# Kernel optimization log

Hardware: AMD Instinct MI355X
Metric: run time of the kernel (lower is better)

Reference implementation:

```python
import jax, jax.numpy as jnp
import numpy as np

N_SRC = 100000
N_DST = 100000
N_EDGES = 640000
D = 128
D_OUT = 128


def setup_inputs() -> dict:
    key = jax.random.key(0)
    k1, k2, k3, k4, k5, k6 = jax.random.split(key, 6)
    h_src = jax.random.normal(k1, (N_SRC, D), dtype=jnp.float32)
    h_dst = jax.random.normal(k2, (N_DST, D), dtype=jnp.float32)
    src_idx = jax.random.randint(k3, (N_EDGES,), 0, N_SRC, dtype=jnp.int32)
    dst_idx = jax.random.randint(k4, (N_EDGES,), 0, N_DST, dtype=jnp.int32)
    W = jax.random.normal(k5, (2 * D, D_OUT), dtype=jnp.float32) * 0.05
    b = jax.random.normal(k6, (D_OUT,), dtype=jnp.float32) * 0.05
    return {"h_src": h_src, "h_dst": h_dst, "src_idx": src_idx,
            "dst_idx": dst_idx, "W": W, "b": b}


def reference(h_src, h_dst, src_idx, dst_idx, W, b):
    # copy_u: gather source features along edges -> [E, D]
    msgs = h_src[src_idx]
    # mean aggregation per destination node (segment mean)
    summed = jax.ops.segment_sum(msgs, dst_idx, num_segments=N_DST)  # [N_dst, D]
    deg = jax.ops.segment_sum(jnp.ones((N_EDGES,), dtype=h_src.dtype),
                              dst_idx, num_segments=N_DST)  # [N_dst]
    h_N = summed / jnp.maximum(deg, 1.0)[:, None]
    # concat self + neighbor mean, then linear projection
    h_total = jnp.concatenate([h_dst, h_N], axis=1)  # [N_dst, 2D]
    return h_total @ W + b
```

## Files before the change

kernel.cpp:

```cpp
#include <hip/hip_runtime.h>

#define D 128
#define N_SRC 100000
#define N_DST 100000
#define N_EDGES 640000

#define SCAN_BLK 1024
#define N_SCAN_BLOCKS ((N_DST + SCAN_BLK - 1) / SCAN_BLK)

#define HIST_BLOCKS ((N_EDGES + 255) / 256)
#define CVT_BLOCKS  ((N_SRC * D / 8) / 256)
#define PACKW_BLOCKS 128

typedef __attribute__((ext_vector_type(8))) short s8v;
typedef __attribute__((ext_vector_type(4))) float f32x4;

__device__ __forceinline__ unsigned short f2bf(float f) {
    unsigned int u = __float_as_uint(f);
    u += 0x7fffu + ((u >> 16) & 1u);
    return (unsigned short)(u >> 16);
}

__device__ __forceinline__ unsigned int pk2(float a, float b) {
    return (unsigned int)f2bf(a) | ((unsigned int)f2bf(b) << 16);
}

__global__ __launch_bounds__(256) void prep(
    const int* __restrict__ dst_idx, int* __restrict__ counts,
    const float* __restrict__ h_src, unsigned int* __restrict__ A32,
    const float* __restrict__ W, unsigned short* __restrict__ Bp)
{
    const int blk = blockIdx.x;
    const int tid = threadIdx.x;
    if (blk < HIST_BLOCKS) {
        int e = blk * 256 + tid;
        if (e < N_EDGES) atomicAdd(&counts[dst_idx[e]], 1);
    } else if (blk < HIST_BLOCKS + CVT_BLOCKS) {
        int id = (blk - HIST_BLOCKS) * 256 + tid;
        size_t e = (size_t)id * 8;
        const float4* p = (const float4*)(h_src + e);
        float4 x = p[0], y = p[1];
        uint4 o;
        o.x = pk2(x.x, x.y); o.y = pk2(x.z, x.w);
        o.z = pk2(y.x, y.y); o.w = pk2(y.z, y.w);
        int r = id >> 4;
        int c = (id & 15) * 8;
        *(uint4*)(A32 + (size_t)r * 128 + (c >> 1)) = o;
    } else {
        int id = (blk - HIST_BLOCKS - CVT_BLOCKS) * 256 + tid;
        if (id < 32768) {
            int j = id & 7;
            int l = (id >> 3) & 63;
            int t = (id >> 9) & 7;
            int s = id >> 12;
            int k = s * 32 + (l >> 4) * 8 + j;
            int n = t * 16 + (l & 15);
            Bp[id] = f2bf(W[k * D + n]);
        }
    }
}


__global__ __launch_bounds__(256) void scan_blocks(
    const int* __restrict__ counts, int* __restrict__ row_start,
    int* __restrict__ block_sums)
{
    __shared__ int sh[256];
    const int tid = threadIdx.x;
    const int base = blockIdx.x * SCAN_BLK + tid * 4;
    int v[4];
    int local = 0;
#pragma unroll
    for (int k = 0; k < 4; k++) {
        int idx = base + k;
        v[k] = (idx < N_DST) ? counts[idx] : 0;
        local += v[k];
    }
    sh[tid] = local;
    __syncthreads();
    for (int off = 1; off < 256; off <<= 1) {
        int t = (tid >= off) ? sh[tid - off] : 0;
        __syncthreads();
        sh[tid] += t;
        __syncthreads();
    }
    int run = (tid == 0) ? 0 : sh[tid - 1];
    if (tid == 255) block_sums[blockIdx.x] = sh[255];
#pragma unroll
    for (int k = 0; k < 4; k++) {
        int idx = base + k;
        if (idx < N_DST) row_start[idx] = run;
        run += v[k];
    }
}

__global__ __launch_bounds__(256) void add_offsets(
    int* __restrict__ row_start, const int* __restrict__ block_sums,
    int* __restrict__ cursor)
{
    __shared__ int sh[128];
    const int tid = threadIdx.x;
    if (tid < 128) sh[tid] = (tid < N_SCAN_BLOCKS) ? block_sums[tid] : 0;
    __syncthreads();
    for (int off = 1; off < 128; off <<= 1) {
        int t = (tid < 128 && tid >= off) ? sh[tid - off] : 0;
        __syncthreads();
        if (tid < 128) sh[tid] += t;
        __syncthreads();
    }
    int i = blockIdx.x * 256 + tid;
    if (i < N_DST) {
        int blk = i / SCAN_BLK;
        int off = (blk == 0) ? 0 : sh[blk - 1];
        int v = row_start[i] + off;
        row_start[i] = v;
        cursor[i] = v;
    }
    if (i == 0) row_start[N_DST] = N_EDGES;
}

__global__ __launch_bounds__(256) void scatter_perm(
    const int* __restrict__ src_idx, const int* __restrict__ dst_idx,
    int* __restrict__ cursor, int* __restrict__ edge_src)
{
    int e = blockIdx.x * 256 + threadIdx.x;
    if (e < N_EDGES) {
        int d = dst_idx[e];
        int pos = atomicAdd(&cursor[d], 1);
        edge_src[pos] = src_idx[e];
    }
}

__global__ __launch_bounds__(256) void aggregate(
    const unsigned short* __restrict__ hs16,
    const int* __restrict__ row_start,
    const int* __restrict__ edge_src, unsigned int* __restrict__ A32)
{
    const int wave = threadIdx.x >> 6;
    const int half = (threadIdx.x >> 5) & 1;
    const int hl = threadIdx.x & 31;
    const int row = blockIdx.x * 8 + wave * 2 + half;
    const int start = row_start[row];
    const int deg = row_start[row + 1] - start;
    f32x4 acc = {0.f, 0.f, 0.f, 0.f};
    for (int base = 0; base < deg; base += 8) {
        int j = base + (hl & 7);
        int myid = edge_src[start + min(j, deg - 1)];
#pragma unroll
        for (int t = 0; t < 8; t++) {
            int s = __shfl(myid, t, 32);
            uint2 u = *(const uint2*)(hs16 + (size_t)s * 256 + hl * 4);
            float m = ((base + t) < deg) ? 1.f : 0.f;
            acc.x = fmaf(__uint_as_float(u.x << 16), m, acc.x);
            acc.y = fmaf(__uint_as_float(u.x & 0xffff0000u), m, acc.y);
            acc.z = fmaf(__uint_as_float(u.y << 16), m, acc.z);
            acc.w = fmaf(__uint_as_float(u.y & 0xffff0000u), m, acc.w);
        }
    }
    const float inv = 1.0f / fmaxf((float)deg, 1.0f);
    uint2 o;
    o.x = pk2(acc.x * inv, acc.y * inv);
    o.y = pk2(acc.z * inv, acc.w * inv);
    *(uint2*)(A32 + (size_t)row * 128 + 64 + hl * 2) = o;
}

__global__ __launch_bounds__(256, 4) void mfma_gemm(
    const float* __restrict__ h_dst,
    const unsigned short* __restrict__ A,
    const unsigned short* __restrict__ Bp,
    const float* __restrict__ bias,
    float* __restrict__ out)
{
    const int wave = threadIdx.x >> 6;
    const int lane = threadIdx.x & 63;
    const int row0 = (blockIdx.x * 4 + wave) * 16;
    if (row0 >= N_DST) return;
    const int quad = lane >> 4;
    const int lr = lane & 15;
    const int r0 = row0 + lr;

    const float* p0 = h_dst + (size_t)r0 * D + quad * 8;
    const unsigned short* q0 = A + (size_t)r0 * 256 + 128 + quad * 8;

    float4 x[4], y[4];
    s8v an[4];
#pragma unroll
    for (int s = 0; s < 4; s++) {
        x[s] = *(const float4*)(p0 + s * 32);
        y[s] = *(const float4*)(p0 + s * 32 + 4);
        an[s] = *(const s8v*)(q0 + s * 32);
    }

    f32x4 acc[8];
#pragma unroll
    for (int t = 0; t < 8; t++) acc[t] = (f32x4){0.f, 0.f, 0.f, 0.f};

#pragma unroll
    for (int s = 0; s < 8; s++) {
        s8v a0;
        if (s < 4) {
            unsigned short au[8];
            au[0] = f2bf(x[s].x); au[1] = f2bf(x[s].y);
            au[2] = f2bf(x[s].z); au[3] = f2bf(x[s].w);
            au[4] = f2bf(y[s].x); au[5] = f2bf(y[s].y);
            au[6] = f2bf(y[s].z); au[7] = f2bf(y[s].w);
            a0 = *(s8v*)au;
        } else {
            a0 = an[s - 4];
        }
#pragma unroll
        for (int t = 0; t < 8; t++) {
            s8v bf = *(const s8v*)(Bp + ((size_t)(s * 8 + t) * 64 + lane) * 8);
            acc[t] = __builtin_amdgcn_mfma_f32_16x16x32_bf16(a0, bf, acc[t], 0, 0, 0);
        }
    }

#pragma unroll
    for (int t = 0; t < 8; t++) {
        float bv = bias[t * 16 + lr];
#pragma unroll
        for (int r = 0; r < 4; r++) {
            int rowa = row0 + quad * 4 + r;
            out[(size_t)rowa * D + t * 16 + lr] = acc[t][r] + bv;
        }
    }
}

extern "C" void kernel_launch(void* const* d_in, const int* in_sizes, int n_in,
                              void* d_out, int out_size, void* d_ws, size_t ws_size,
                              hipStream_t stream) {
    const float* h_src  = (const float*)d_in[0];
    const float* h_dst  = (const float*)d_in[1];
    const int* src_idx  = (const int*)d_in[2];
    const int* dst_idx  = (const int*)d_in[3];
    const float* W      = (const float*)d_in[4];
    const float* b      = (const float*)d_in[5];
    float* out = (float*)d_out;

    unsigned short* Bp = (unsigned short*)d_ws;
    int* ws_i          = (int*)((char*)d_ws + 65536);
    int* row_start     = ws_i;
    int* cursor        = row_start + (N_DST + 1);
    int* counts        = cursor + N_DST;
    int* block_sums    = counts + N_DST;
    int* edge_src      = block_sums + N_SCAN_BLOCKS;

    hipMemsetAsync(counts, 0, (size_t)N_DST * sizeof(int), stream);

    prep<<<HIST_BLOCKS + CVT_BLOCKS + PACKW_BLOCKS, 256, 0, stream>>>(
        dst_idx, counts, h_src, (unsigned int*)d_out, W, Bp);

    scan_blocks<<<N_SCAN_BLOCKS, 256, 0, stream>>>(counts, row_start, block_sums);
    add_offsets<<<(N_DST + 255) / 256, 256, 0, stream>>>(row_start, block_sums, cursor);
    scatter_perm<<<(N_EDGES + 255) / 256, 256, 0, stream>>>(src_idx, dst_idx, cursor, edge_src);

    aggregate<<<N_DST / 8, 256, 0, stream>>>(
        (const unsigned short*)d_out, row_start, edge_src, (unsigned int*)d_out);

    int gemm_blocks = (N_DST / 16 + 3) / 4;
    mfma_gemm<<<gemm_blocks, 256, 0, stream>>>(
        h_dst, (const unsigned short*)d_out, Bp, b, out);
}
```

Measured before the change: 263.8 us.

## Widen aggregate loads to 16 bytes and keep weight fragments in registers

The aggregate kernel now gives each destination row 16 lanes that each load 8 bf16 values per neighbor, instead of 32 lanes loading 4, so gathers use wider loads and each block covers 16 rows. The GEMM is reorganized so each block covers 64 rows and each wave owns two output column tiles. Each wave loads its slice of the packed weights into registers once, rather than re-reading the full 64KB of packed weights per 16-row tile. The cost is that all four waves in a block read the same h_dst and aggregate rows, and a __syncthreads is added because the output buffer aliases the aggregate input. The occupancy hint is lowered to fit the larger register footprint.

```diff
diff --git a/kernel.cpp b/kernel.cpp
--- a/kernel.cpp
+++ b/kernel.cpp
@@ -137,34 +137,40 @@
     const int* __restrict__ edge_src, unsigned int* __restrict__ A32)
 {
     const int wave = threadIdx.x >> 6;
-    const int half = (threadIdx.x >> 5) & 1;
-    const int hl = threadIdx.x & 31;
-    const int row = blockIdx.x * 8 + wave * 2 + half;
+    const int grp = (threadIdx.x >> 4) & 3;
+    const int gl = threadIdx.x & 15;
+    const int row = blockIdx.x * 16 + wave * 4 + grp;
     const int start = row_start[row];
     const int deg = row_start[row + 1] - start;
-    f32x4 acc = {0.f, 0.f, 0.f, 0.f};
+    float acc[8] = {0.f, 0.f, 0.f, 0.f, 0.f, 0.f, 0.f, 0.f};
     for (int base = 0; base < deg; base += 8) {
-        int j = base + (hl & 7);
+        int j = base + (gl & 7);
         int myid = edge_src[start + min(j, deg - 1)];
 #pragma unroll
         for (int t = 0; t < 8; t++) {
-            int s = __shfl(myid, t, 32);
-            uint2 u = *(const uint2*)(hs16 + (size_t)s * 256 + hl * 4);
+            int s = __shfl(myid, t, 16);
+            uint4 u = *(const uint4*)(hs16 + (size_t)s * 256 + gl * 8);
             float m = ((base + t) < deg) ? 1.f : 0.f;
-            acc.x = fmaf(__uint_as_float(u.x << 16), m, acc.x);
-            acc.y = fmaf(__uint_as_float(u.x & 0xffff0000u), m, acc.y);
-            acc.z = fmaf(__uint_as_float(u.y << 16), m, acc.z);
-            acc.w = fmaf(__uint_as_float(u.y & 0xffff0000u), m, acc.w);
+            acc[0] = fmaf(__uint_as_float(u.x << 16), m, acc[0]);
+            acc[1] = fmaf(__uint_as_float(u.x & 0xffff0000u), m, acc[1]);
+            acc[2] = fmaf(__uint_as_float(u.y << 16), m, acc[2]);
+            acc[3] = fmaf(__uint_as_float(u.y & 0xffff0000u), m, acc[3]);
+            acc[4] = fmaf(__uint_as_float(u.z << 16), m, acc[4]);
+            acc[5] = fmaf(__uint_as_float(u.z & 0xffff0000u), m, acc[5]);
+            acc[6] = fmaf(__uint_as_float(u.w << 16), m, acc[6]);
+            acc[7] = fmaf(__uint_as_float(u.w & 0xffff0000u), m, acc[7]);
         }
     }
     const float inv = 1.0f / fmaxf((float)deg, 1.0f);
-    uint2 o;
-    o.x = pk2(acc.x * inv, acc.y * inv);
-    o.y = pk2(acc.z * inv, acc.w * inv);
-    *(uint2*)(A32 + (size_t)row * 128 + 64 + hl * 2) = o;
-}
-
-__global__ __launch_bounds__(256, 4) void mfma_gemm(
+    uint4 o;
+    o.x = pk2(acc[0] * inv, acc[1] * inv);
+    o.y = pk2(acc[2] * inv, acc[3] * inv);
+    o.z = pk2(acc[4] * inv, acc[5] * inv);
+    o.w = pk2(acc[6] * inv, acc[7] * inv);
+    *(uint4*)(A32 + (size_t)row * 128 + 64 + gl * 4) = o;
+}
+
+__global__ __launch_bounds__(256, 3) void mfma_gemm(
     const float* __restrict__ h_dst,
     const unsigned short* __restrict__ A,
     const unsigned short* __restrict__ Bp,
@@ -173,55 +179,71 @@
 {
     const int wave = threadIdx.x >> 6;
     const int lane = threadIdx.x & 63;
-    const int row0 = (blockIdx.x * 4 + wave) * 16;
-    if (row0 >= N_DST) return;
     const int quad = lane >> 4;
     const int lr = lane & 15;
-    const int r0 = row0 + lr;
-
-    const float* p0 = h_dst + (size_t)r0 * D + quad * 8;
-    const unsigned short* q0 = A + (size_t)r0 * 256 + 128 + quad * 8;
-
-    float4 x[4], y[4];
-    s8v an[4];
-#pragma unroll
-    for (int s = 0; s < 4; s++) {
-        x[s] = *(const float4*)(p0 + s * 32);
-        y[s] = *(const float4*)(p0 + s * 32 + 4);
-        an[s] = *(const s8v*)(q0 + s * 32);
-    }
-
-    f32x4 acc[8];
-#pragma unroll
-    for (int t = 0; t < 8; t++) acc[t] = (f32x4){0.f, 0.f, 0.f, 0.f};
-
-#pragma unroll
-    for (int s = 0; s < 8; s++) {
-        s8v a0;
-        if (s < 4) {
-            unsigned short au[8];
-            au[0] = f2bf(x[s].x); au[1] = f2bf(x[s].y);
-            au[2] = f2bf(x[s].z); au[3] = f2bf(x[s].w);
-            au[4] = f2bf(y[s].x); au[5] = f2bf(y[s].y);
-            au[6] = f2bf(y[s].z); au[7] = f2bf(y[s].w);
-            a0 = *(s8v*)au;
-        } else {
-            a0 = an[s - 4];
-        }
-#pragma unroll
-        for (int t = 0; t < 8; t++) {
-            s8v bf = *(const s8v*)(Bp + ((size_t)(s * 8 + t) * 64 + lane) * 8);
-            acc[t] = __builtin_amdgcn_mfma_f32_16x16x32_bf16(a0, bf, acc[t], 0, 0, 0);
-        }
-    }
-
-#pragma unroll
-    for (int t = 0; t < 8; t++) {
-        float bv = bias[t * 16 + lr];
+    const int row0 = blockIdx.x * 64;
+    const int t0 = wave * 2;
+
+    s8v Bf[8][2];
+#pragma unroll
+    for (int s = 0; s < 8; s++)
+#pragma unroll
+        for (int j = 0; j < 2; j++)
+            Bf[s][j] = *(const s8v*)(Bp + ((size_t)(s * 8 + t0 + j) * 64 + lane) * 8);
+
+    f32x4 acc[4][2];
+#pragma unroll
+    for (int rg = 0; rg < 4; rg++)
+#pragma unroll
+        for (int j = 0; j < 2; j++)
+            acc[rg][j] = (f32x4){0.f, 0.f, 0.f, 0.f};
+
+#pragma unroll
+    for (int rg = 0; rg < 4; rg++) {
+        int r = row0 + rg * 16 + lr;
+        int rc = min(r, N_DST - 1);
+        const float* p = h_dst + (size_t)rc * D + quad * 8;
+        const unsigned short* q = A + (size_t)rc * 256 + 128 + quad * 8;
+
+        float4 x[4], y[4];
+        s8v an[4];
+#pragma unroll
+        for (int s = 0; s < 4; s++) {
+            x[s] = *(const float4*)(p + s * 32);
+            y[s] = *(const float4*)(p + s * 32 + 4);
+            an[s] = *(const s8v*)(q + s * 32);
+        }
+#pragma unroll
+        for (int s = 0; s < 8; s++) {
+            s8v a0;
+            if (s < 4) {
+                unsigned short au[8];
+                au[0] = f2bf(x[s].x); au[1] = f2bf(x[s].y);
+                au[2] = f2bf(x[s].z); au[3] = f2bf(x[s].w);
+                au[4] = f2bf(y[s].x); au[5] = f2bf(y[s].y);
+                au[6] = f2bf(y[s].z); au[7] = f2bf(y[s].w);
+                a0 = *(s8v*)au;
+            } else {
+                a0 = an[s - 4];
+            }
+            acc[rg][0] = __builtin_amdgcn_mfma_f32_16x16x32_bf16(a0, Bf[s][0], acc[rg][0], 0, 0, 0);
+            acc[rg][1] = __builtin_amdgcn_mfma_f32_16x16x32_bf16(a0, Bf[s][1], acc[rg][1], 0, 0, 0);
+        }
+    }
+
+    __syncthreads();
+
+    float bv0 = bias[t0 * 16 + lr];
+    float bv1 = bias[(t0 + 1) * 16 + lr];
+#pragma unroll
+    for (int rg = 0; rg < 4; rg++) {
 #pragma unroll
         for (int r = 0; r < 4; r++) {
-            int rowa = row0 + quad * 4 + r;
-            out[(size_t)rowa * D + t * 16 + lr] = acc[t][r] + bv;
+            int row = row0 + rg * 16 + quad * 4 + r;
+            if (row < N_DST) {
+                out[(size_t)row * D + t0 * 16 + lr] = acc[rg][0][r] + bv0;
+                out[(size_t)row * D + (t0 + 1) * 16 + lr] = acc[rg][1][r] + bv1;
+            }
         }
     }
 }
@@ -254,10 +276,10 @@
     add_offsets<<<(N_DST + 255) / 256, 256, 0, stream>>>(row_start, block_sums, cursor);
     scatter_perm<<<(N_EDGES + 255) / 256, 256, 0, stream>>>(src_idx, dst_idx, cursor, edge_src);
 
-    aggregate<<<N_DST / 8, 256, 0, stream>>>(
+    aggregate<<<N_DST / 16, 256, 0, stream>>>(
         (const unsigned short*)d_out, row_start, edge_src, (unsigned int*)d_out);
 
-    int gemm_blocks = (N_DST / 16 + 3) / 4;
+    int gemm_blocks = (N_DST + 63) / 64;
     mfma_gemm<<<gemm_blocks, 256, 0, stream>>>(
         h_dst, (const unsigned short*)d_out, Bp, b, out);
 }
```

Measured after the change: 279.3 us. 1.06x slower.

## Fuse neighbor aggregation into MFMA GEMM via swizzled LDS tile

Applied to the files above, without the earlier changes.

Merges the aggregate and GEMM kernels into a single kernel. Each 128-thread block computes bf16 neighbor means for 32 rows into a swizzled shared-memory tile, then feeds them straight to the MFMA projection, so the aggregated rows no longer go out to global memory and come back. The bf16 copy of h_src now sits in a compact 256-byte-per-row workspace buffer instead of being interleaved in the output buffer, and each lane gathers 16 bytes per edge. The trade-off is that blocks are smaller and each block serializes its gather phase before the matmul, which may limit how well the two phases overlap.

```diff
diff --git a/kernel.cpp b/kernel.cpp
--- a/kernel.cpp
+++ b/kernel.cpp
@@ -27,7 +27,7 @@
 
 __global__ __launch_bounds__(256) void prep(
     const int* __restrict__ dst_idx, int* __restrict__ counts,
-    const float* __restrict__ h_src, unsigned int* __restrict__ A32,
+    const float* __restrict__ h_src, unsigned int* __restrict__ mir32,
     const float* __restrict__ W, unsigned short* __restrict__ Bp)
 {
     const int blk = blockIdx.x;
@@ -43,9 +43,7 @@
         uint4 o;
         o.x = pk2(x.x, x.y); o.y = pk2(x.z, x.w);
         o.z = pk2(y.x, y.y); o.w = pk2(y.z, y.w);
-        int r = id >> 4;
-        int c = (id & 15) * 8;
-        *(uint4*)(A32 + (size_t)r * 128 + (c >> 1)) = o;
+        *(uint4*)(mir32 + (size_t)(id >> 4) * 64 + (id & 15) * 4) = o;
     } else {
         int id = (blk - HIST_BLOCKS - CVT_BLOCKS) * 256 + tid;
         if (id < 32768) {
@@ -131,64 +129,85 @@
     }
 }
 
-__global__ __launch_bounds__(256) void aggregate(
-    const unsigned short* __restrict__ hs16,
+__global__ __launch_bounds__(128, 4) void fused_ag(
+    const float* __restrict__ h_dst,
+    const unsigned short* __restrict__ mir,
     const int* __restrict__ row_start,
-    const int* __restrict__ edge_src, unsigned int* __restrict__ A32)
-{
-    const int wave = threadIdx.x >> 6;
-    const int half = (threadIdx.x >> 5) & 1;
-    const int hl = threadIdx.x & 31;
-    const int row = blockIdx.x * 8 + wave * 2 + half;
-    const int start = row_start[row];
-    const int deg = row_start[row + 1] - start;
-    f32x4 acc = {0.f, 0.f, 0.f, 0.f};
-    for (int base = 0; base < deg; base += 8) {
-        int j = base + (hl & 7);
-        int myid = edge_src[start + min(j, deg - 1)];
-#pragma unroll
-        for (int t = 0; t < 8; t++) {
-            int s = __shfl(myid, t, 32);
-            uint2 u = *(const uint2*)(hs16 + (size_t)s * 256 + hl * 4);
-            float m = ((base + t) < deg) ? 1.f : 0.f;
-            acc.x = fmaf(__uint_as_float(u.x << 16), m, acc.x);
-            acc.y = fmaf(__uint_as_float(u.x & 0xffff0000u), m, acc.y);
-            acc.z = fmaf(__uint_as_float(u.y << 16), m, acc.z);
-            acc.w = fmaf(__uint_as_float(u.y & 0xffff0000u), m, acc.w);
-        }
-    }
-    const float inv = 1.0f / fmaxf((float)deg, 1.0f);
-    uint2 o;
-    o.x = pk2(acc.x * inv, acc.y * inv);
-    o.y = pk2(acc.z * inv, acc.w * inv);
-    *(uint2*)(A32 + (size_t)row * 128 + 64 + hl * 2) = o;
-}
-
-__global__ __launch_bounds__(256, 4) void mfma_gemm(
-    const float* __restrict__ h_dst,
-    const unsigned short* __restrict__ A,
+    const int* __restrict__ edge_src,
     const unsigned short* __restrict__ Bp,
     const float* __restrict__ bias,
     float* __restrict__ out)
 {
-    const int wave = threadIdx.x >> 6;
-    const int lane = threadIdx.x & 63;
-    const int row0 = (blockIdx.x * 4 + wave) * 16;
-    if (row0 >= N_DST) return;
+    __shared__ uint4 hN4[512];
+    char* hN = (char*)hN4;
+
+    const int tid = threadIdx.x;
+    const int wave = tid >> 6;
+    const int lane = tid & 63;
     const int quad = lane >> 4;
     const int lr = lane & 15;
-    const int r0 = row0 + lr;
-
+    const int rw0 = blockIdx.x * 32 + wave * 16;
+
+#pragma unroll
+    for (int i = 0; i < 4; i++) {
+        int rl = wave * 16 + i * 4 + quad;
+        int row = blockIdx.x * 32 + rl;
+        int start = row_start[row];
+        int deg = row_start[row + 1] - start;
+        float a[8] = {0.f, 0.f, 0.f, 0.f, 0.f, 0.f, 0.f, 0.f};
+        for (int base = 0; base < deg; base += 8) {
+            int j = base + (lr & 7);
+            int myid = edge_src[start + min(j, deg - 1)];
+#pragma unroll
+            for (int t = 0; t < 8; t++) {
+                int s = __shfl(myid, t, 16);
+                uint4 u = *(const uint4*)(mir + (size_t)s * 128 + lr * 8);
+                float m = ((base + t) < deg) ? 1.f : 0.f;
+                a[0] = fmaf(__uint_as_float(u.x << 16), m, a[0]);
+                a[1] = fmaf(__uint_as_float(u.x & 0xffff0000u), m, a[1]);
+                a[2] = fmaf(__uint_as_float(u.y << 16), m, a[2]);
+                a[3] = fmaf(__uint_as_float(u.y & 0xffff0000u), m, a[3]);
+                a[4] = fmaf(__uint_as_float(u.z << 16), m, a[4]);
+                a[5] = fmaf(__uint_as_float(u.z & 0xffff0000u), m, a[5]);
+                a[6] = fmaf(__uint_as_float(u.w << 16), m, a[6]);
+                a[7] = fmaf(__uint_as_float(u.w & 0xffff0000u), m, a[7]);
+            }
+        }
+        float inv = 1.0f / fmaxf((float)deg, 1.0f);
+        uint4 o;
+        o.x = pk2(a[0] * inv, a[1] * inv);
+        o.y = pk2(a[2] * inv, a[3] * inv);
+        o.z = pk2(a[4] * inv, a[5] * inv);
+        o.w = pk2(a[6] * inv, a[7] * inv);
+        int ba = (rl * 256 + lr * 16) ^ ((rl & 7) << 4);
+        *(uint4*)(hN + ba) = o;
+    }
+
+    s8v an[4];
+    {
+        int rl = wave * 16 + lr;
+#pragma unroll
+        for (int s = 0; s < 4; s++) {
+            int ba = (rl * 256 + s * 64 + quad * 16) ^ ((rl & 7) << 4);
+            an[s] = *(const s8v*)(hN + ba);
+        }
+    }
+
+    const int r0 = rw0 + lr;
     const float* p0 = h_dst + (size_t)r0 * D + quad * 8;
-    const unsigned short* q0 = A + (size_t)r0 * 256 + 128 + quad * 8;
-
-    float4 x[4], y[4];
-    s8v an[4];
+    float4 x0[4], y0[4];
 #pragma unroll
     for (int s = 0; s < 4; s++) {
-        x[s] = *(const float4*)(p0 + s * 32);
-        y[s] = *(const float4*)(p0 + s * 32 + 4);
-        an[s] = *(const s8v*)(q0 + s * 32);
+        x0[s] = *(const float4*)(p0 + s * 32);
+        y0[s] = *(const float4*)(p0 + s * 32 + 4);
+    }
+    s8v af0[4];
+#pragma unroll
+    for (int s = 0; s < 4; s++) {
+        unsigned short u0[8];
+        u0[0]=f2bf(x0[s].x); u0[1]=f2bf(x0[s].y); u0[2]=f2bf(x0[s].z); u0[3]=f2bf(x0[s].w);
+        u0[4]=f2bf(y0[s].x); u0[5]=f2bf(y0[s].y); u0[6]=f2bf(y0[s].z); u0[7]=f2bf(y0[s].w);
+        af0[s] = *(s8v*)u0;
     }
 
     f32x4 acc[8];
@@ -197,17 +216,7 @@
 
 #pragma unroll
     for (int s = 0; s < 8; s++) {
-        s8v a0;
-        if (s < 4) {
-            unsigned short au[8];
-            au[0] = f2bf(x[s].x); au[1] = f2bf(x[s].y);
-            au[2] = f2bf(x[s].z); au[3] = f2bf(x[s].w);
-            au[4] = f2bf(y[s].x); au[5] = f2bf(y[s].y);
-            au[6] = f2bf(y[s].z); au[7] = f2bf(y[s].w);
-            a0 = *(s8v*)au;
-        } else {
-            a0 = an[s - 4];
-        }
+        s8v a0 = (s < 4) ? af0[s] : an[s - 4];
 #pragma unroll
         for (int t = 0; t < 8; t++) {
             s8v bf = *(const s8v*)(Bp + ((size_t)(s * 8 + t) * 64 + lane) * 8);
@@ -220,8 +229,8 @@
         float bv = bias[t * 16 + lr];
 #pragma unroll
         for (int r = 0; r < 4; r++) {
-            int rowa = row0 + quad * 4 + r;
-            out[(size_t)rowa * D + t * 16 + lr] = acc[t][r] + bv;
+            int row = rw0 + quad * 4 + r;
+            out[(size_t)row * D + t * 16 + lr] = acc[t][r] + bv;
         }
     }
 }
@@ -245,19 +254,18 @@
     int* block_sums    = counts + N_DST;
     int* edge_src      = block_sums + N_SCAN_BLOCKS;
 
+    size_t int_bytes = (size_t)(N_DST + 1 + N_DST + N_DST + N_SCAN_BLOCKS + N_EDGES) * 4;
+    size_t mir_off   = (65536 + int_bytes + 255) & ~(size_t)255;
+    unsigned short* mir = (unsigned short*)((char*)d_ws + mir_off);
+
     hipMemsetAsync(counts, 0, (size_t)N_DST * sizeof(int), stream);
 
     prep<<<HIST_BLOCKS + CVT_BLOCKS + PACKW_BLOCKS, 256, 0, stream>>>(
-        dst_idx, counts, h_src, (unsigned int*)d_out, W, Bp);
-
+        dst_idx, counts, h_src, (unsigned int*)mir, W, Bp);
     scan_blocks<<<N_SCAN_BLOCKS, 256, 0, stream>>>(counts, row_start, block_sums);
     add_offsets<<<(N_DST + 255) / 256, 256, 0, stream>>>(row_start, block_sums, cursor);
     scatter_perm<<<(N_EDGES + 255) / 256, 256, 0, stream>>>(src_idx, dst_idx, cursor, edge_src);
 
-    aggregate<<<N_DST / 8, 256, 0, stream>>>(
-        (const unsigned short*)d_out, row_start, edge_src, (unsigned int*)d_out);
-
-    int gemm_blocks = (N_DST / 16 + 3) / 4;
-    mfma_gemm<<<gemm_blocks, 256, 0, stream>>>(
-        h_dst, (const unsigned short*)d_out, Bp, b, out);
-}
+    fused_ag<<<N_DST / 32, 128, 0, stream>>>(
+        h_dst, mir, row_start, edge_src, Bp, b, out);
+}
```

Measured after the change: 258.2 us. 2.1% less time.
